# Kernel tuning notes

Hardware: AMD Instinct MI355X
Metric: run time of the kernel (lower is better)

Reference implementation:

```python
import jax, jax.numpy as jnp
import numpy as np

B, S, D, H, HD, NU, T = 64, 512, 256, 4, 64, 100000, 24


def setup_inputs() -> dict:
    key = jax.random.key(0)
    ks = jax.random.split(key, 13)
    return {
        "timeslot_embedded": jax.random.normal(ks[0], (T, D), jnp.float32),
        "user": jax.random.randint(ks[1], (B,), 0, NU, dtype=jnp.int64) if jax.config.jax_enable_x64 else jax.random.randint(ks[1], (B,), 0, NU, dtype=jnp.int32),
        "hour": jax.random.randint(ks[2], (B, S), 0, T, dtype=jnp.int32),
        "hour_mask": jax.random.randint(ks[3], (B, S, T), 0, 2, dtype=jnp.int32),
        "user_pref": jax.random.normal(ks[4], (NU, D), jnp.float32) * 0.02,
        "Wq": jax.random.normal(ks[5], (H, HD, 2 * D), jnp.float32) * 0.02,
        "bq": jnp.zeros((H, HD), jnp.float32),
        "Wk": jax.random.normal(ks[6], (H, HD, D), jnp.float32) * 0.02,
        "bk": jnp.zeros((H, HD), jnp.float32),
        "Wv": jax.random.normal(ks[7], (H, HD, D), jnp.float32) * 0.02,
        "bv": jnp.zeros((H, HD), jnp.float32),
        "Wu": jax.random.normal(ks[8], (D, D), jnp.float32) * 0.02,
        "bu": jnp.zeros((D,), jnp.float32),
    }


def reference(timeslot_embedded, user, hour, hour_mask, user_pref,
              Wq, bq, Wk, bk, Wv, bv, Wu, bu):
    b, s = hour.shape
    n = b * s
    # per-token features
    user_feat = jnp.broadcast_to(user_pref[user][:, None, :], (b, s, D)).reshape(n, D)
    time_feat = timeslot_embedded[hour.reshape(n)]          # [N, D]
    query = jnp.concatenate([user_feat, time_feat], axis=-1)  # [N, 2D]
    # all heads at once (equivalent to the per-head Linear loop)
    q = jnp.einsum('nd,hkd->nhk', query, Wq) + bq[None]               # [N, H, HD]
    k = jnp.einsum('td,hkd->htk', timeslot_embedded, Wk) + bk[:, None, :]  # [H, T, HD]
    v = jnp.einsum('td,hkd->htk', timeslot_embedded, Wv) + bv[:, None, :]  # [H, T, HD]
    scale = 1.0 / np.sqrt(HD).astype(np.float32)
    scores = jnp.einsum('nhk,htk->nht', q, k) * scale                 # [N, H, T]
    mask = hour_mask.reshape(n, T)[:, None, :]                        # [N, 1, T]
    scores = jnp.where(mask == 1, -jnp.inf, scores)
    attn = jax.nn.softmax(scores, axis=-1)
    out = jnp.einsum('nht,htk->nhk', attn, v).reshape(n, H * HD)      # concat heads
    out = out @ Wu.T + bu
    return out.reshape(b, s, D)
```

## Files before the change

kernel.cpp:

```cpp
#include <hip/hip_runtime.h>
#include <hip/hip_bf16.h>

#define QU_OFF   0
#define KK_OFF   16384
#define ET_OFF   22528
#define VWB_OFF  24832

typedef __attribute__((ext_vector_type(8))) short bf16x8;
typedef __attribute__((ext_vector_type(4))) float f32x4;
typedef __attribute__((ext_vector_type(4))) int   i32x4;

__device__ __forceinline__ unsigned short f2bf(float f) {
    unsigned u = __builtin_bit_cast(unsigned, f);
    return (unsigned short)((u + 0x7FFFu + ((u >> 16) & 1u)) >> 16);
}
__device__ __forceinline__ unsigned packbf(float a, float b) {
    return (unsigned)f2bf(a) | ((unsigned)f2bf(b) << 16);
}
__device__ __forceinline__ bf16x8 cvt8(float4 f0, float4 f1) {
    int4 v = make_int4(packbf(f0.x, f0.y), packbf(f0.z, f0.w),
                       packbf(f1.x, f1.y), packbf(f1.z, f1.w));
    return __builtin_bit_cast(bf16x8, v);
}
__device__ __forceinline__ float dot4(float4 a, float4 b, float s) {
    return fmaf(a.x, b.x, fmaf(a.y, b.y, fmaf(a.z, b.z, fmaf(a.w, b.w, s))));
}
__device__ __forceinline__ float dot4v(f32x4 a, f32x4 b, float s) {
    return fmaf(a[0], b[0], fmaf(a[1], b[1], fmaf(a[2], b[2], fmaf(a[3], b[3], s))));
}


__global__ __launch_bounds__(256) void precomp(
    const float* __restrict__ ts, const int* __restrict__ user,
    const float* __restrict__ user_pref,
    const float* __restrict__ Wq, const float* __restrict__ bq,
    const float* __restrict__ Wk, const float* __restrict__ bk,
    const float* __restrict__ Wv, const float* __restrict__ bv,
    const float* __restrict__ Wu, float* __restrict__ ws)
{
    __shared__ unsigned sA[4096];
    __shared__ float sM1[32 * 68];
    __shared__ float sM2[32 * 68];
    int tid = threadIdx.x, blk = blockIdx.x;
    int w = tid >> 6, l = tid & 63;
    int eo = (l >> 4) * 8;

    if (blk < 16) {
        int q = blk >> 2, co = (blk & 3) * 64, b0 = q * 16;
        int col = co + w * 16 + (l & 15);
        float4 fb[8][2];
        #pragma unroll
        for (int kt = 0; kt < 8; ++kt) {
            const float* Bp = Wq + (size_t)col * 512 + kt * 32 + eo;
            fb[kt][0] = *(const float4*)Bp; fb[kt][1] = *(const float4*)(Bp + 4);
        }
        for (int u = tid; u < 512; u += 256) {
            int r = u >> 5, e0 = (u & 31) * 8;
            const float* src = user_pref + (size_t)user[b0 + r] * 256 + e0;
            float4 f0 = *(const float4*)src, f1 = *(const float4*)(src + 4);
            unsigned* dst = &sA[(((e0 >> 5) * 2) * 64 + (r & 15) + 16 * ((e0 >> 3) & 3)) * 4];
            dst[0] = packbf(f0.x, f0.y); dst[1] = packbf(f0.z, f0.w);
            dst[2] = packbf(f1.x, f1.y); dst[3] = packbf(f1.z, f1.w);
        }
        __syncthreads();
        f32x4 acc = (f32x4)0.f;
        #pragma unroll
        for (int kt = 0; kt < 8; ++kt) {
            bf16x8 afr = __builtin_bit_cast(bf16x8, *(const int4*)&sA[((kt * 2) * 64 + l) * 4]);
            acc = __builtin_amdgcn_mfma_f32_16x16x32_bf16(afr, cvt8(fb[kt][0], fb[kt][1]), acc, 0, 0, 0);
        }
        int row = (l >> 4) * 4;
        #pragma unroll
        for (int r = 0; r < 4; ++r)
            ws[QU_OFF + (size_t)(b0 + row + r) * 256 + col] = acc[r];
        return;
    }

    if (blk < 20) {
        int h = blk - 16;
        int j = h * 64 + w * 16 + (l & 15);
        float4 fa[8][2], fc[8][2];
        #pragma unroll
        for (int kt = 0; kt < 8; ++kt) {
            const float* Bq = Wq + (size_t)j * 512 + 256 + kt * 32 + eo;
            const float* Bk = Wk + (size_t)j * 256 + kt * 32 + eo;
            fa[kt][0] = *(const float4*)Bq; fa[kt][1] = *(const float4*)(Bq + 4);
            fc[kt][0] = *(const float4*)Bk; fc[kt][1] = *(const float4*)(Bk + 4);
        }
        for (int u = tid; u < 768; u += 256) {
            int r = u >> 5, e0 = (u & 31) * 8;
            const float* src = ts + r * 256 + e0;
            float4 f0 = *(const float4*)src, f1 = *(const float4*)(src + 4);
            unsigned* dst = &sA[(((e0 >> 5) * 2 + (r >> 4)) * 64 + (r & 15) + 16 * ((e0 >> 3) & 3)) * 4];
            dst[0] = packbf(f0.x, f0.y); dst[1] = packbf(f0.z, f0.w);
            dst[2] = packbf(f1.x, f1.y); dst[3] = packbf(f1.z, f1.w);
        }
        __syncthreads();
        f32x4 aca[2] = {(f32x4)0.f, (f32x4)0.f};
        f32x4 acb[2] = {(f32x4)0.f, (f32x4)0.f};
        #pragma unroll
        for (int kt = 0; kt < 8; ++kt) {
            bf16x8 bq8 = cvt8(fa[kt][0], fa[kt][1]);
            bf16x8 bk8 = cvt8(fc[kt][0], fc[kt][1]);
            #pragma unroll
            for (int mt = 0; mt < 2; ++mt) {
                bf16x8 afr = __builtin_bit_cast(bf16x8, *(const int4*)&sA[((kt * 2 + mt) * 64 + l) * 4]);
                aca[mt] = __builtin_amdgcn_mfma_f32_16x16x32_bf16(afr, bq8, aca[mt], 0, 0, 0);
                acb[mt] = __builtin_amdgcn_mfma_f32_16x16x32_bf16(afr, bk8, acb[mt], 0, 0, 0);
            }
        }
        float bqv = bq[j], bkv = bk[j];
        int hd = w * 16 + (l & 15);
        #pragma unroll
        for (int mt = 0; mt < 2; ++mt) {
            int t0 = mt * 16 + (l >> 4) * 4;
            #pragma unroll
            for (int r = 0; r < 4; ++r) {
                int t = t0 + r;
                if (t < 24) {
                    sM1[t * 68 + hd] = aca[mt][r] + bqv;
                    float kv = acb[mt][r] + bkv;
                    sM2[t * 68 + hd] = kv;
                    ws[KK_OFF + (h * 24 + t) * 64 + hd] = kv;
                }
            }
        }
        __syncthreads();
        for (int u = tid; u < 576; u += 256) {
            int tp = u / 24, t = u - tp * 24;
            const float4* qp4 = (const float4*)&sM1[tp * 68];
            const float4* kp4 = (const float4*)&sM2[t * 68];
            float s = 0.f;
            #pragma unroll
            for (int i = 0; i < 16; ++i) s = dot4(qp4[i], kp4[i], s);
            ws[ET_OFF + tp * 96 + h * 24 + t] = expf(s * 0.125f);
        }
        return;
    }

    {
        int h = blk - 20;
        int jv = h * 64 + w * 16 + (l & 15);
        float4 fv[8][2];
        #pragma unroll
        for (int kt = 0; kt < 8; ++kt) {
            const float* Bv = Wv + (size_t)jv * 256 + kt * 32 + eo;
            fv[kt][0] = *(const float4*)Bv; fv[kt][1] = *(const float4*)(Bv + 4);
        }
        float4 fu[2][4][2];
        #pragma unroll
        for (int kt2 = 0; kt2 < 2; ++kt2) {
            int k0 = kt2 * 32 + eo;
            #pragma unroll
            for (int q = 0; q < 4; ++q) {
                int d = (w * 4 + q) * 16 + (l & 15);
                const float* Bu = Wu + (size_t)d * 256 + h * 64 + k0;
                fu[kt2][q][0] = *(const float4*)Bu; fu[kt2][q][1] = *(const float4*)(Bu + 4);
            }
        }
        for (int u = tid; u < 768; u += 256) {
            int r = u >> 5, e0 = (u & 31) * 8;
            const float* src = ts + r * 256 + e0;
            float4 f0 = *(const float4*)src, f1 = *(const float4*)(src + 4);
            unsigned* dst = &sA[(((e0 >> 5) * 2 + (r >> 4)) * 64 + (r & 15) + 16 * ((e0 >> 3) & 3)) * 4];
            dst[0] = packbf(f0.x, f0.y); dst[1] = packbf(f0.z, f0.w);
            dst[2] = packbf(f1.x, f1.y); dst[3] = packbf(f1.z, f1.w);
        }
        __syncthreads();
        f32x4 acv[2] = {(f32x4)0.f, (f32x4)0.f};
        #pragma unroll
        for (int kt = 0; kt < 8; ++kt) {
            bf16x8 bv8 = cvt8(fv[kt][0], fv[kt][1]);
            #pragma unroll
            for (int mt = 0; mt < 2; ++mt) {
                bf16x8 afr = __builtin_bit_cast(bf16x8, *(const int4*)&sA[((kt * 2 + mt) * 64 + l) * 4]);
                acv[mt] = __builtin_amdgcn_mfma_f32_16x16x32_bf16(afr, bv8, acv[mt], 0, 0, 0);
            }
        }
        float bvv = bv[jv];
        int hd = w * 16 + (l & 15);
        #pragma unroll
        for (int mt = 0; mt < 2; ++mt) {
            int t0 = mt * 16 + (l >> 4) * 4;
            #pragma unroll
            for (int r = 0; r < 4; ++r)
                if (t0 + r < 24) sM1[(t0 + r) * 68 + hd] = acv[mt][r] + bvv;
        }
        __syncthreads();
        f32x4 ac2[2][4];
        #pragma unroll
        for (int mt = 0; mt < 2; ++mt)
            #pragma unroll
            for (int q = 0; q < 4; ++q) ac2[mt][q] = (f32x4)0.f;
        #pragma unroll
        for (int kt2 = 0; kt2 < 2; ++kt2) {
            int k0 = kt2 * 32 + eo;
            bf16x8 a2[2];
            #pragma unroll
            for (int mt = 0; mt < 2; ++mt) {
                int m = mt * 16 + (l & 15);
                float4 g0 = *(const float4*)&sM1[m * 68 + k0];
                float4 g1 = *(const float4*)&sM1[m * 68 + k0 + 4];
                a2[mt] = cvt8(g0, g1);
            }
            #pragma unroll
            for (int q = 0; q < 4; ++q) {
                bf16x8 bu8 = cvt8(fu[kt2][q][0], fu[kt2][q][1]);
                #pragma unroll
                for (int mt = 0; mt < 2; ++mt)
                    ac2[mt][q] = __builtin_amdgcn_mfma_f32_16x16x32_bf16(a2[mt], bu8, ac2[mt][q], 0, 0, 0);
            }
        }
        unsigned* vwb = (unsigned*)(ws + VWB_OFF);
        #pragma unroll
        for (int mt = 0; mt < 2; ++mt) {
            int t0 = mt * 16 + (l >> 4) * 4;
            if (t0 < 24) {
                #pragma unroll
                for (int q = 0; q < 4; ++q) {
                    int d = (w * 4 + q) * 16 + (l & 15);
                    #pragma unroll
                    for (int pp = 0; pp < 2; ++pp) {
                        int ht = h * 24 + t0 + pp * 2;
                        unsigned pk = packbf(ac2[mt][q][pp * 2], ac2[mt][q][pp * 2 + 1]);
                        int ktC = ht >> 5, ntC = d >> 4;
                        int lgC = (ht >> 3) & 3, jhC = (ht & 7) >> 1;
                        vwb[(ktC * 16 + ntC) * 256 + ((d & 15) + 16 * lgC) * 4 + jhC] = pk;
                    }
                }
            }
        }
    }
}

__global__ __launch_bounds__(256, 2) void attn_mfma(
    const int* __restrict__ hour, const int* __restrict__ hour_mask,
    const float* __restrict__ ws, const float* __restrict__ bu,
    float* __restrict__ out)
{
    const float* ET = ws + ET_OFF;
    __shared__ int4 A_lds[12 * 64];
    __shared__ float EU_s[96];
    __shared__ __align__(16) float stg[4 * 1088];
    int tid = threadIdx.x, w = tid >> 6, l = tid & 63;
    int nb = blockIdx.x * 64;
    int b = nb >> 9;

    int tok = tid >> 2, h = tid & 3, n = nb + tok;
    int th = hour[n];
    const i32x4* mp = (const i32x4*)(hour_mask + (long long)n * 24);
    i32x4 msk[6];
    #pragma unroll
    for (int q = 0; q < 6; ++q) msk[q] = __builtin_nontemporal_load(mp + q);
    const int4* Bg = (const int4*)(ws + VWB_OFF);
    int4 breg[12];
    #pragma unroll
    for (int kt = 0; kt < 3; ++kt)
        #pragma unroll
        for (int q = 0; q < 4; ++q)
            breg[kt * 4 + q] = Bg[(kt * 16 + w * 4 + q) * 64 + l];
    if (tid < 96) {
        const f32x4* qp = (const f32x4*)(ws + QU_OFF + b * 256 + (tid / 24) * 64);
        const f32x4* kp = (const f32x4*)(ws + KK_OFF + tid * 64);
        float s = 0.f;
        #pragma unroll
        for (int i = 0; i < 16; ++i) s = dot4v(qp[i], kp[i], s);
        EU_s[tid] = expf(s * 0.125f);
    }
    const f32x4* ETp = (const f32x4*)(ET + th * 96 + h * 24);
    f32x4 fET[6];
    #pragma unroll
    for (int q = 0; q < 6; ++q) fET[q] = ETp[q];
    __syncthreads();
    {
        const f32x4* EUp = (const f32x4*)(EU_s + h * 24);
        float p[24]; float ssum = 0.f;
        #pragma unroll
        for (int q = 0; q < 6; ++q) {
            f32x4 e = EUp[q]; f32x4 f = fET[q]; i32x4 mm = msk[q];
            float v0 = (mm[0] != 0) ? 0.f : e[0] * f[0];
            float v1 = (mm[1] != 0) ? 0.f : e[1] * f[1];
            float v2 = (mm[2] != 0) ? 0.f : e[2] * f[2];
            float v3 = (mm[3] != 0) ? 0.f : e[3] * f[3];
            p[q*4+0] = v0; p[q*4+1] = v1; p[q*4+2] = v2; p[q*4+3] = v3;
            ssum += (v0 + v1) + (v2 + v3);
        }
        float r = 1.0f / ssum;
        int mt = tok >> 4, tl = tok & 15;
        #pragma unroll
        for (int tp = 0; tp < 12; ++tp) {
            int ht = h * 24 + tp * 2;
            unsigned pack = packbf(p[tp*2] * r, p[tp*2+1] * r);
            int kt = ht >> 5, lg = (ht >> 3) & 3, jh = (ht & 7) >> 1;
            ((unsigned*)A_lds)[((kt * 4 + mt) * 64 + tl + 16 * lg) * 4 + jh] = pack;
        }
    }
    __syncthreads();
    bf16x8 afr[3][4];
    #pragma unroll
    for (int kt = 0; kt < 3; ++kt)
        #pragma unroll
        for (int q = 0; q < 4; ++q)
            afr[kt][q] = __builtin_bit_cast(bf16x8, A_lds[(kt * 4 + q) * 64 + l]);
    f32x4 acc[4][4];
    #pragma unroll
    for (int mt = 0; mt < 4; ++mt)
        #pragma unroll
        for (int q = 0; q < 4; ++q) acc[mt][q] = (f32x4)0.f;
    #pragma unroll
    for (int kt = 0; kt < 3; ++kt)
        #pragma unroll
        for (int mt = 0; mt < 4; ++mt)
            #pragma unroll
            for (int q = 0; q < 4; ++q)
                acc[mt][q] = __builtin_amdgcn_mfma_f32_16x16x32_bf16(
                    afr[kt][mt], __builtin_bit_cast(bf16x8, breg[kt * 4 + q]),
                    acc[mt][q], 0, 0, 0);
    float* sp = stg + w * 1088;
    int rr = l >> 2, cg = l & 3;
    f32x4 bu4[4];
    #pragma unroll
    for (int i = 0; i < 4; ++i)
        bu4[i] = *(const f32x4*)(bu + w * 64 + i * 16 + cg * 4);
    #pragma unroll
    for (int mt = 0; mt < 4; ++mt) {
        #pragma unroll
        for (int q = 0; q < 4; ++q)
            #pragma unroll
            for (int r = 0; r < 4; ++r)
                sp[((l >> 4) * 4 + r) * 68 + q * 16 + (l & 15)] = acc[mt][q][r];
        float* orow = out + (size_t)(nb + mt * 16 + rr) * 256 + w * 64;
        #pragma unroll
        for (int i = 0; i < 4; ++i) {
            f32x4 v = *(const f32x4*)(sp + rr * 68 + i * 16 + cg * 4);
            v = v + bu4[i];
            __builtin_nontemporal_store(v, (f32x4*)(orow + i * 16 + cg * 4));
        }
    }
}

extern "C" void kernel_launch(void* const* d_in, const int* in_sizes, int n_in,
                              void* d_out, int out_size, void* d_ws, size_t ws_size,
                              hipStream_t stream)
{
    const float* ts        = (const float*)d_in[0];
    const int*   user      = (const int*)  d_in[1];
    const int*   hour      = (const int*)  d_in[2];
    const int*   hour_mask = (const int*)  d_in[3];
    const float* user_pref = (const float*)d_in[4];
    const float* Wq        = (const float*)d_in[5];
    const float* bq        = (const float*)d_in[6];
    const float* Wk        = (const float*)d_in[7];
    const float* bk        = (const float*)d_in[8];
    const float* Wv        = (const float*)d_in[9];
    const float* bv        = (const float*)d_in[10];
    const float* Wu        = (const float*)d_in[11];
    const float* bu        = (const float*)d_in[12];
    float* ws  = (float*)d_ws;
    float* out = (float*)d_out;

    hipLaunchKernelGGL(precomp, dim3(24), dim3(256), 0, stream,
                       ts, user, user_pref, Wq, bq, Wk, bk, Wv, bv, Wu, ws);
    hipLaunchKernelGGL(attn_mfma, dim3(512), dim3(256), 0, stream,
                       hour, hour_mask, ws, bu, out);
}
```

Measured before the change: 24.22 us.

## Halve attention block to 32 tokens with 2 waves and pipelined B-fragment loads

The attention kernel now runs 1024 blocks of 128 threads, each handling 32 tokens. Each of the 2 waves computes a 32x128 output tile instead of the earlier 64x64 per-wave tile. Weight (B) fragments are loaded per k-step into two alternating register buffers, so the next loads overlap with the MFMAs of the current step. The output bias is staged once in LDS. The aim is more blocks per CU and better latency hiding, at the cost of twice the B-fragment loads across the grid and more accumulator registers per wave.

```diff
diff --git a/kernel.cpp b/kernel.cpp
--- a/kernel.cpp
+++ b/kernel.cpp
@@ -233,17 +233,18 @@
     }
 }
 
-__global__ __launch_bounds__(256, 2) void attn_mfma(
+__global__ __launch_bounds__(128, 2) void attn_mfma(
     const int* __restrict__ hour, const int* __restrict__ hour_mask,
     const float* __restrict__ ws, const float* __restrict__ bu,
     float* __restrict__ out)
 {
     const float* ET = ws + ET_OFF;
-    __shared__ int4 A_lds[12 * 64];
+    __shared__ int4 A_lds[6 * 64];
     __shared__ float EU_s[96];
-    __shared__ __align__(16) float stg[4 * 1088];
+    __shared__ float bu_s[256];
+    __shared__ __align__(16) float stg[2 * 16 * 132];
     int tid = threadIdx.x, w = tid >> 6, l = tid & 63;
-    int nb = blockIdx.x * 64;
+    int nb = blockIdx.x * 32;
     int b = nb >> 9;
 
     int tok = tid >> 2, h = tid & 3, n = nb + tok;
@@ -252,13 +253,11 @@
     i32x4 msk[6];
     #pragma unroll
     for (int q = 0; q < 6; ++q) msk[q] = __builtin_nontemporal_load(mp + q);
+    if (tid < 64) *(f32x4*)&bu_s[tid * 4] = *(const f32x4*)(bu + tid * 4);
     const int4* Bg = (const int4*)(ws + VWB_OFF);
-    int4 breg[12];
-    #pragma unroll
-    for (int kt = 0; kt < 3; ++kt)
-        #pragma unroll
-        for (int q = 0; q < 4; ++q)
-            breg[kt * 4 + q] = Bg[(kt * 16 + w * 4 + q) * 64 + l];
+    int4 br_a[8], br_b[8];
+    #pragma unroll
+    for (int q = 0; q < 8; ++q) br_a[q] = Bg[(w * 8 + q) * 64 + l];
     if (tid < 96) {
         const f32x4* qp = (const f32x4*)(ws + QU_OFF + b * 256 + (tid / 24) * 64);
         const f32x4* kp = (const f32x4*)(ws + KK_OFF + tid * 64);
@@ -292,48 +291,57 @@
             int ht = h * 24 + tp * 2;
             unsigned pack = packbf(p[tp*2] * r, p[tp*2+1] * r);
             int kt = ht >> 5, lg = (ht >> 3) & 3, jh = (ht & 7) >> 1;
-            ((unsigned*)A_lds)[((kt * 4 + mt) * 64 + tl + 16 * lg) * 4 + jh] = pack;
+            ((unsigned*)A_lds)[((kt * 2 + mt) * 64 + tl + 16 * lg) * 4 + jh] = pack;
         }
     }
     __syncthreads();
-    bf16x8 afr[3][4];
+    bf16x8 afr[3][2];
     #pragma unroll
     for (int kt = 0; kt < 3; ++kt)
         #pragma unroll
-        for (int q = 0; q < 4; ++q)
-            afr[kt][q] = __builtin_bit_cast(bf16x8, A_lds[(kt * 4 + q) * 64 + l]);
-    f32x4 acc[4][4];
-    #pragma unroll
-    for (int mt = 0; mt < 4; ++mt)
-        #pragma unroll
-        for (int q = 0; q < 4; ++q) acc[mt][q] = (f32x4)0.f;
-    #pragma unroll
-    for (int kt = 0; kt < 3; ++kt)
-        #pragma unroll
-        for (int mt = 0; mt < 4; ++mt)
-            #pragma unroll
-            for (int q = 0; q < 4; ++q)
-                acc[mt][q] = __builtin_amdgcn_mfma_f32_16x16x32_bf16(
-                    afr[kt][mt], __builtin_bit_cast(bf16x8, breg[kt * 4 + q]),
-                    acc[mt][q], 0, 0, 0);
-    float* sp = stg + w * 1088;
+        for (int mt = 0; mt < 2; ++mt)
+            afr[kt][mt] = __builtin_bit_cast(bf16x8, A_lds[(kt * 2 + mt) * 64 + l]);
+    f32x4 acc[2][8];
+    #pragma unroll
+    for (int mt = 0; mt < 2; ++mt)
+        #pragma unroll
+        for (int q = 0; q < 8; ++q) acc[mt][q] = (f32x4)0.f;
+    #pragma unroll
+    for (int q = 0; q < 8; ++q) br_b[q] = Bg[(16 + w * 8 + q) * 64 + l];
+    #pragma unroll
+    for (int mt = 0; mt < 2; ++mt)
+        #pragma unroll
+        for (int q = 0; q < 8; ++q)
+            acc[mt][q] = __builtin_amdgcn_mfma_f32_16x16x32_bf16(
+                afr[0][mt], __builtin_bit_cast(bf16x8, br_a[q]), acc[mt][q], 0, 0, 0);
+    #pragma unroll
+    for (int q = 0; q < 8; ++q) br_a[q] = Bg[(32 + w * 8 + q) * 64 + l];
+    #pragma unroll
+    for (int mt = 0; mt < 2; ++mt)
+        #pragma unroll
+        for (int q = 0; q < 8; ++q)
+            acc[mt][q] = __builtin_amdgcn_mfma_f32_16x16x32_bf16(
+                afr[1][mt], __builtin_bit_cast(bf16x8, br_b[q]), acc[mt][q], 0, 0, 0);
+    #pragma unroll
+    for (int mt = 0; mt < 2; ++mt)
+        #pragma unroll
+        for (int q = 0; q < 8; ++q)
+            acc[mt][q] = __builtin_amdgcn_mfma_f32_16x16x32_bf16(
+                afr[2][mt], __builtin_bit_cast(bf16x8, br_a[q]), acc[mt][q], 0, 0, 0);
+    float* sp = stg + w * (16 * 132);
     int rr = l >> 2, cg = l & 3;
-    f32x4 bu4[4];
-    #pragma unroll
-    for (int i = 0; i < 4; ++i)
-        bu4[i] = *(const f32x4*)(bu + w * 64 + i * 16 + cg * 4);
-    #pragma unroll
-    for (int mt = 0; mt < 4; ++mt) {
-        #pragma unroll
-        for (int q = 0; q < 4; ++q)
+    #pragma unroll
+    for (int mt = 0; mt < 2; ++mt) {
+        #pragma unroll
+        for (int q = 0; q < 8; ++q)
             #pragma unroll
             for (int r = 0; r < 4; ++r)
-                sp[((l >> 4) * 4 + r) * 68 + q * 16 + (l & 15)] = acc[mt][q][r];
-        float* orow = out + (size_t)(nb + mt * 16 + rr) * 256 + w * 64;
-        #pragma unroll
-        for (int i = 0; i < 4; ++i) {
-            f32x4 v = *(const f32x4*)(sp + rr * 68 + i * 16 + cg * 4);
-            v = v + bu4[i];
+                sp[((l >> 4) * 4 + r) * 132 + q * 16 + (l & 15)] = acc[mt][q][r];
+        float* orow = out + (size_t)(nb + mt * 16 + rr) * 256 + w * 128;
+        #pragma unroll
+        for (int i = 0; i < 8; ++i) {
+            f32x4 v = *(const f32x4*)(sp + rr * 132 + i * 16 + cg * 4);
+            v = v + *(const f32x4*)(&bu_s[w * 128 + i * 16 + cg * 4]);
             __builtin_nontemporal_store(v, (f32x4*)(orow + i * 16 + cg * 4));
         }
     }
@@ -361,6 +369,6 @@
 
     hipLaunchKernelGGL(precomp, dim3(24), dim3(256), 0, stream,
                        ts, user, user_pref, Wq, bq, Wk, bk, Wv, bv, Wu, ws);
-    hipLaunchKernelGGL(attn_mfma, dim3(512), dim3(256), 0, stream,
+    hipLaunchKernelGGL(attn_mfma, dim3(1024), dim3(128), 0, stream,
                        hour, hour_mask, ws, bu, out);
 }
```

Measured after the change: 27.05 us. 11.7% more time.
